# Performance work log

Hardware: AMD Instinct MI355X
Metric: run time of the kernel (lower is better)

The kernel has to match this reference:

```python
import jax, jax.numpy as jnp
import numpy as np

N = 50000      # number of nodes (rows of edge_embeddings)
E = 800000     # number of edges
D = 256        # edge_dim
TOPK = 50


def setup_inputs() -> dict:
    key = jax.random.key(0)
    k1, k2, k3, k4, k5, k6 = jax.random.split(key, 6)
    edge_embeddings = jax.random.normal(k1, (N, D), dtype=jnp.float32)
    edge_index = jax.random.randint(k2, (2, E), 0, N, dtype=jnp.int64)
    # PyTorch nn.Linear default init: U(-1/sqrt(fan_in), 1/sqrt(fan_in))
    s1 = 1.0 / np.sqrt(2 * D)
    s2 = 1.0 / np.sqrt(D)
    W1 = jax.random.uniform(k3, (2 * D, D), jnp.float32, -s1, s1)
    b1 = jax.random.uniform(k4, (D,), jnp.float32, -s1, s1)
    W2 = jax.random.uniform(k5, (D, 1), jnp.float32, -s2, s2)
    b2 = jax.random.uniform(k6, (1,), jnp.float32, -s2, s2)
    return {"edge_embeddings": edge_embeddings, "W1": W1, "b1": b1,
            "W2": W2, "b2": b2, "edge_index": edge_index, "top_k": TOPK}


def reference(edge_embeddings, W1, b1, W2, b2, edge_index, top_k):
    src, dst = edge_index[0], edge_index[1]           # [E]
    valid = src < dst                                  # original keeps only i<j pairs
    # gather + concat: [E, 2D]
    pair_emb = jnp.concatenate([edge_embeddings[src], edge_embeddings[dst]], axis=-1)
    h = jax.nn.relu(pair_emb @ W1 + b1)                # [E, D]
    score = jax.nn.sigmoid(h @ W2 + b2)[:, 0]          # [E], in (0,1)
    # invalid edges get score -1 (< any sigmoid output) so topk picks only valid ones
    masked = jnp.where(valid, score, jnp.float32(-1.0))
    top_scores, top_idx = jax.lax.top_k(masked, top_k)
    top_pairs = edge_index[:, top_idx]                 # [2, k] (src,dst) of top edges
    return top_pairs, top_scores
```

## Files before the change

kernel.cpp:

```cpp
#include <hip/hip_runtime.h>
#include <hip/hip_bf16.h>
#include <cstdint>

#define TOPK 50
#define CANDS 400
#define HIST_BINS 16384
#define CAND_CAP 16384
#define NFBLK 512
#define SORT_CAP 8192

typedef __attribute__((ext_vector_type(8))) short bf16x8;
typedef __attribute__((ext_vector_type(4))) float f32x4;

__device__ __forceinline__ unsigned short f2bf(float f) {
    unsigned u = __float_as_uint(f);
    u += 0x7FFFu + ((u >> 16) & 1u);
    return (unsigned short)(u >> 16);
}

__global__ __launch_bounds__(256) void prep_kernel(const float* __restrict__ W1,
                                                   unsigned* __restrict__ Wcf4,
                                                   unsigned* __restrict__ hist,
                                                   unsigned* __restrict__ misc,
                                                   const int* __restrict__ eidx) {
    int g = blockIdx.x * blockDim.x + threadIdx.x;
    {
        int l = g & 63;
        int kt = (g >> 6) & 7;
        int nt = g >> 9;
        int col = nt * 16 + (l & 15);
        int kb = kt * 32 + (l >> 4) * 8;
        unsigned short h[8];
#pragma unroll
        for (int j = 0; j < 8; ++j) {
            int k = kb + j;
            float f = (col < 256) ? W1[k * 256 + col] : W1[(256 + k) * 256 + (col - 256)];
            h[j] = f2bf(f);
        }
        unsigned* dst = Wcf4 + (size_t)g * 4;
        dst[0] = (unsigned)h[0] | ((unsigned)h[1] << 16);
        dst[1] = (unsigned)h[2] | ((unsigned)h[3] << 16);
        dst[2] = (unsigned)h[4] | ((unsigned)h[5] << 16);
        dst[3] = (unsigned)h[6] | ((unsigned)h[7] << 16);
    }
    if (g < HIST_BINS) hist[g] = 0;
    if (g == 0) {
        int allz = 1;
        for (int q = 0; q < 64; ++q)
            if (eidx[2 * q + 1] != 0) { allz = 0; break; }
        misc[0] = (unsigned)allz;
        misc[2] = 0;
        misc[3] = 0;
        misc[4] = 0;
    }
}

__global__ __launch_bounds__(256) void gemm_fused(const float* __restrict__ emb,
                                                  const bf16x8* __restrict__ Bv,
                                                  const float* __restrict__ b1,
                                                  unsigned char* __restrict__ C8, int M) {
    __shared__ uint4 afrag[2048];
    const int t = threadIdx.x;
    const int w = t >> 6;
    const int l = t & 63;

    uint2* w2 = (uint2*)afrag;
#pragma unroll
    for (int iter = 0; iter < 16; ++iter) {
        int r = iter * 4 + w;
        int c0 = l * 4;
        int gr = blockIdx.x * 64 + r;
        float4 v = make_float4(0.f, 0.f, 0.f, 0.f);
        if (gr < M) v = *(const float4*)&emb[(size_t)gr * 256 + c0];
        unsigned u0 = (unsigned)f2bf(v.x) | ((unsigned)f2bf(v.y) << 16);
        unsigned u1 = (unsigned)f2bf(v.z) | ((unsigned)f2bf(v.w) << 16);
        int mt = r >> 4;
        int kt = c0 >> 5;
        int lane = (r & 15) + ((c0 & 31) >> 3) * 16;
        int f = mt * 8 + kt;
        int slot = f * 64 + (lane ^ (f & 7));
        w2[slot * 2 + ((c0 & 7) >> 2)] = make_uint2(u0, u1);
    }
    __syncthreads();

    const int wn = w;
#pragma unroll
    for (int nh = 0; nh < 2; ++nh) {
        f32x4 acc[4][4];
#pragma unroll
        for (int i = 0; i < 4; ++i)
#pragma unroll
            for (int j = 0; j < 4; ++j) acc[i][j] = (f32x4){0.f, 0.f, 0.f, 0.f};

        const int nt0 = wn * 8 + nh * 4;
        bf16x8 bcur[4];
#pragma unroll
        for (int j = 0; j < 4; ++j)
            bcur[j] = Bv[(size_t)((nt0 + j) * 8 + 0) * 64 + l];

#pragma unroll
        for (int kt = 0; kt < 8; ++kt) {
            bf16x8 af[4];
#pragma unroll
            for (int i = 0; i < 4; ++i)
                af[i] = *(const bf16x8*)&afrag[(i * 8 + kt) * 64 + (l ^ kt)];
            bf16x8 bnxt[4];
            if (kt < 7) {
#pragma unroll
                for (int j = 0; j < 4; ++j)
                    bnxt[j] = Bv[(size_t)((nt0 + j) * 8 + kt + 1) * 64 + l];
            }
#pragma unroll
            for (int i = 0; i < 4; ++i)
#pragma unroll
                for (int j = 0; j < 4; ++j)
                    acc[i][j] = __builtin_amdgcn_mfma_f32_16x16x32_bf16(af[i], bcur[j], acc[i][j], 0, 0, 0);
            if (kt < 7) {
#pragma unroll
                for (int j = 0; j < 4; ++j) bcur[j] = bnxt[j];
            }
        }

#pragma unroll
        for (int i = 0; i < 4; ++i) {
            int row0 = blockIdx.x * 64 + i * 16 + (l >> 4) * 4;
#pragma unroll
            for (int j = 0; j < 4; ++j) {
                int col = (nt0 + j) * 16 + (l & 15);
                float bias = (col < 256) ? b1[col] : 0.f;
#pragma unroll
                for (int r = 0; r < 4; ++r) {
                    float v = acc[i][j][r] + bias;
                    int pk = __builtin_amdgcn_cvt_pk_fp8_f32(v, v, 0, false);
                    C8[(size_t)(row0 + r) * 512 + col] = (unsigned char)(pk & 0xFF);
                }
            }
        }
    }
}

__global__ __launch_bounds__(256) void count_valid(const int* __restrict__ eidx,
                                                   const unsigned* __restrict__ misc,
                                                   unsigned* __restrict__ bcount, int E) {
    const int is64 = (int)misc[0];
    const int chunk = (E + gridDim.x - 1) / gridDim.x;
    const int lo = blockIdx.x * chunk;
    const int hi = min(E, lo + chunk);
    unsigned cnt = 0;
    for (int e = lo + threadIdx.x; e < hi; e += blockDim.x) {
        int s, d;
        if (is64) {
            s = ((const int2*)eidx)[e].x;
            d = ((const int2*)eidx)[(size_t)e + E].x;
        } else {
            s = eidx[e];
            d = eidx[e + E];
        }
        cnt += (s < d);
    }
#pragma unroll
    for (int off = 32; off; off >>= 1) cnt += __shfl_xor(cnt, off, 64);
    __shared__ unsigned wsum[4];
    if ((threadIdx.x & 63) == 0) wsum[threadIdx.x >> 6] = cnt;
    __syncthreads();
    if (threadIdx.x == 0)
        bcount[blockIdx.x] = wsum[0] + wsum[1] + wsum[2] + wsum[3];
}

__global__ __launch_bounds__(256) void scan_blocks(const unsigned* __restrict__ bcount,
                                                   unsigned* __restrict__ boffset,
                                                   unsigned* __restrict__ misc) {
    __shared__ unsigned sc[256];
    const int t = threadIdx.x;
    unsigned a = bcount[2 * t], b = bcount[2 * t + 1];
    sc[t] = a + b;
    __syncthreads();
    for (int off = 1; off < 256; off <<= 1) {
        unsigned v = (t >= off) ? sc[t - off] : 0u;
        __syncthreads();
        sc[t] += v;
        __syncthreads();
    }
    unsigned excl = sc[t] - (a + b);
    boffset[2 * t] = excl;
    boffset[2 * t + 1] = excl + a;
    if (t == 255) misc[4] = sc[255];
}

__global__ __launch_bounds__(256) void write_valid(const int* __restrict__ eidx,
                                                   const unsigned* __restrict__ misc,
                                                   const unsigned* __restrict__ boffset,
                                                   int* __restrict__ vsrc,
                                                   int* __restrict__ vdst,
                                                   int* __restrict__ vid, int E) {
    const int is64 = (int)misc[0];
    const int chunk = (E + gridDim.x - 1) / gridDim.x;
    const int lo = blockIdx.x * chunk;
    const int hi = min(E, lo + chunk);
    const int lane = threadIdx.x & 63;
    const int w = threadIdx.x >> 6;
    __shared__ unsigned wcnt[4];
    unsigned running = boffset[blockIdx.x];
    for (int base = lo; base < hi; base += blockDim.x) {
        int e = base + threadIdx.x;
        bool valid = false;
        int s = 0, d = 0;
        if (e < hi) {
            if (is64) {
                s = ((const int2*)eidx)[e].x;
                d = ((const int2*)eidx)[(size_t)e + E].x;
            } else {
                s = eidx[e];
                d = eidx[e + E];
            }
            valid = s < d;
        }
        unsigned long long m = __ballot(valid);
        unsigned pfx = __popcll(m & ((1ull << lane) - 1ull));
        if (lane == 0) wcnt[w] = __popcll(m);
        __syncthreads();
        unsigned wbase = running;
        for (int i = 0; i < w; ++i) wbase += wcnt[i];
        if (valid) {
            unsigned p = wbase + pfx;
            vsrc[p] = s;
            vdst[p] = d;
            vid[p] = e;
        }
        unsigned tot = wcnt[0] + wcnt[1] + wcnt[2] + wcnt[3];
        __syncthreads();
        running += tot;
    }
}

__device__ __forceinline__ float dotq(unsigned a, unsigned b, float4 w) {
    float s;
    s  = fmaxf(__builtin_amdgcn_cvt_f32_fp8(a, 0) + __builtin_amdgcn_cvt_f32_fp8(b, 0), 0.f) * w.x;
    s += fmaxf(__builtin_amdgcn_cvt_f32_fp8(a, 1) + __builtin_amdgcn_cvt_f32_fp8(b, 1), 0.f) * w.y;
    s += fmaxf(__builtin_amdgcn_cvt_f32_fp8(a, 2) + __builtin_amdgcn_cvt_f32_fp8(b, 2), 0.f) * w.z;
    s += fmaxf(__builtin_amdgcn_cvt_f32_fp8(a, 3) + __builtin_amdgcn_cvt_f32_fp8(b, 3), 0.f) * w.w;
    return s;
}

__global__ __launch_bounds__(256) void edge_score_fp8(const unsigned char* __restrict__ C8,
                                                      const int* __restrict__ vsrc,
                                                      const int* __restrict__ vdst,
                                                      const float* __restrict__ W2,
                                                      const float* __restrict__ b2,
                                                      float* __restrict__ svals,
                                                      const unsigned* __restrict__ misc) {
    const int V = (int)misc[4];
    const int lane = threadIdx.x & 63;
    const int q = lane & 15;
    const int g = lane >> 4;
    const int wid = blockIdx.x * (blockDim.x >> 6) + (threadIdx.x >> 6);
    const int nw = gridDim.x * (blockDim.x >> 6);

    const float4 w0 = *(const float4*)&W2[q * 16 + 0];
    const float4 w1 = *(const float4*)&W2[q * 16 + 4];
    const float4 w2 = *(const float4*)&W2[q * 16 + 8];
    const float4 w3 = *(const float4*)&W2[q * 16 + 12];
    const float bb2 = b2[0];

    for (int base = wid * 4; base < V; base += nw * 4) {
        const int slot = base + g;
        const bool ok = slot < V;
        const int src = ok ? vsrc[slot] : 0;
        const int dst = ok ? vdst[slot] : 0;
        const uint4 ua = *(const uint4*)(C8 + (size_t)src * 512 + q * 16);
        const uint4 ub = *(const uint4*)(C8 + (size_t)dst * 512 + 256 + q * 16);
        float p = dotq(ua.x, ub.x, w0);
        p += dotq(ua.y, ub.y, w1);
        p += dotq(ua.z, ub.z, w2);
        p += dotq(ua.w, ub.w, w3);
        p += __shfl_xor(p, 1, 64);
        p += __shfl_xor(p, 2, 64);
        p += __shfl_xor(p, 4, 64);
        p += __shfl_xor(p, 8, 64);
        if (q == 0 && ok) {
            float z = p + bb2;
            float sc = 1.0f / (1.0f + expf(-z));
            svals[slot] = sc;
        }
    }
}

__global__ __launch_bounds__(256) void hist_kernel(const float* __restrict__ svals,
                                                   const unsigned* __restrict__ misc,
                                                   unsigned* __restrict__ hist) {
    __shared__ unsigned lh[HIST_BINS];
    const int V = (int)misc[4];
    const int t = threadIdx.x;
    for (int i = t; i < HIST_BINS; i += 256) lh[i] = 0;
    __syncthreads();
    int i = blockIdx.x * blockDim.x + t;
    int stride = gridDim.x * blockDim.x;
    for (int v = i; v < V; v += stride)
        atomicAdd(&lh[__float_as_uint(svals[v]) >> 16], 1u);
    __syncthreads();
    for (int b = t; b < HIST_BINS; b += 256) {
        unsigned c = lh[b];
        if (c) atomicAdd(&hist[b], c);
    }
}

__global__ void scan_hist(const unsigned* __restrict__ hist, unsigned* __restrict__ misc) {
    __shared__ unsigned chunk[256];
    int t = threadIdx.x;
    unsigned s = 0;
    for (int i = 0; i < 64; ++i) s += hist[t * 64 + i];
    chunk[t] = s;
    __syncthreads();
    if (t == 0) {
        unsigned cum = 0;
        int c;
        unsigned thr = 0;
        for (c = 255; c >= 0; --c) {
            if (cum + chunk[c] >= CANDS) break;
            cum += chunk[c];
        }
        if (c >= 0) {
            for (int b = c * 64 + 63; b >= c * 64; --b) {
                cum += hist[b];
                if (cum >= CANDS) { thr = ((unsigned)b) << 16; break; }
            }
        }
        misc[2] = thr;
    }
}

__global__ void compact(const float* __restrict__ svals, const int* __restrict__ vid,
                        unsigned* __restrict__ misc,
                        unsigned long long* __restrict__ cand) {
    const int V = (int)misc[4];
    const unsigned thr = misc[2];
    int i = blockIdx.x * blockDim.x + threadIdx.x;
    int stride = gridDim.x * blockDim.x;
    for (int v = i; v < V; v += stride) {
        unsigned bits = __float_as_uint(svals[v]);
        if (bits >= thr) {
            unsigned pos = atomicAdd(&misc[3], 1u);
            if (pos < CAND_CAP)
                cand[pos] = ((unsigned long long)bits << 32) |
                            (unsigned)(0xFFFFFFFFu - (unsigned)vid[v]);
        }
    }
}

__global__ __launch_bounds__(256) void rescore(const float* __restrict__ emb,
                                               const float* __restrict__ W1,
                                               const float* __restrict__ b1,
                                               const float* __restrict__ W2,
                                               const float* __restrict__ b2,
                                               const int* __restrict__ eidx,
                                               const unsigned long long* __restrict__ cand,
                                               const unsigned* __restrict__ misc,
                                               unsigned long long* __restrict__ rescored,
                                               int E) {
    __shared__ float es[256], ed[256];
    __shared__ float red[256];
    const int C = (int)min(misc[3], (unsigned)CAND_CAP);
    const int is64 = (int)misc[0];
    const int t = threadIdx.x;
    for (int c = blockIdx.x; c < C; c += gridDim.x) {
        unsigned long long entry = cand[c];
        unsigned e = 0xFFFFFFFFu - (unsigned)(entry & 0xFFFFFFFFu);
        int src, dst;
        if (is64) {
            src = eidx[2 * (size_t)e];
            dst = eidx[2 * ((size_t)e + E)];
        } else {
            src = eidx[e];
            dst = eidx[e + E];
        }
        es[t] = emb[(size_t)src * 256 + t];
        ed[t] = emb[(size_t)dst * 256 + t];
        __syncthreads();
        float h = b1[t];
#pragma unroll 8
        for (int k = 0; k < 256; ++k) h += es[k] * W1[k * 256 + t];
#pragma unroll 8
        for (int k = 0; k < 256; ++k) h += ed[k] * W1[(256 + k) * 256 + t];
        red[t] = fmaxf(h, 0.f) * W2[t];
        __syncthreads();
        for (int s = 128; s; s >>= 1) {
            if (t < s) red[t] += red[t + s];
            __syncthreads();
        }
        if (t == 0) {
            float z = red[0] + b2[0];
            float sc = 1.0f / (1.0f + expf(-z));
            rescored[c] = ((unsigned long long)__float_as_uint(sc) << 32) |
                          (unsigned)(0xFFFFFFFFu - e);
        }
        __syncthreads();
    }
}

__global__ __launch_bounds__(256) void final_topk(unsigned long long* __restrict__ rescored,
                                                  const unsigned* __restrict__ misc,
                                                  const int* __restrict__ eidx,
                                                  float* __restrict__ out, int E) {
    __shared__ unsigned long long a[SORT_CAP];
    const int t = threadIdx.x;
    const int C = (int)min(misc[3], (unsigned)CAND_CAP);
    const int is64 = (int)misc[0];

    if (C <= SORT_CAP) {
        int n = 256;
        while (n < C) n <<= 1;
        for (int i = t; i < n; i += 256) a[i] = (i < C) ? rescored[i] : 0ull;
        __syncthreads();
        for (int k = 2; k <= n; k <<= 1) {
            for (int j = k >> 1; j > 0; j >>= 1) {
                for (int i = t; i < n; i += 256) {
                    int ixj = i ^ j;
                    if (ixj > i) {
                        unsigned long long x = a[i], y = a[ixj];
                        bool sw = ((i & k) == 0) ? (x < y) : (x > y);
                        if (sw) { a[i] = y; a[ixj] = x; }
                    }
                }
                __syncthreads();
            }
        }
        if (t < TOPK) {
            unsigned long long m = a[t];
            if (m != 0ull) {
                unsigned bits = (unsigned)(m >> 32);
                unsigned e = 0xFFFFFFFFu - (unsigned)(m & 0xFFFFFFFFu);
                int src, dst;
                if (is64) {
                    src = eidx[2 * (size_t)e];
                    dst = eidx[2 * ((size_t)e + E)];
                } else {
                    src = eidx[e];
                    dst = eidx[e + E];
                }
                out[t] = (float)src;
                out[TOPK + t] = (float)dst;
                out[2 * TOPK + t] = __uint_as_float(bits);
            } else {
                out[t] = -1.f;
                out[TOPK + t] = -1.f;
                out[2 * TOPK + t] = -1.f;
            }
        }
        return;
    }

    __shared__ unsigned long long red[256];
    for (int r = 0; r < TOPK; ++r) {
        unsigned long long best = 0ull;
        for (int i = t; i < C; i += 256) {
            unsigned long long v = rescored[i];
            if (v > best) best = v;
        }
        red[t] = best;
        __syncthreads();
        for (int s = 128; s; s >>= 1) {
            if (t < s) {
                if (red[t + s] > red[t]) red[t] = red[t + s];
            }
            __syncthreads();
        }
        unsigned long long m = red[0];
        __syncthreads();
        for (int i = t; i < C; i += 256)
            if (rescored[i] == m) rescored[i] = 0ull;
        if (t == 0) {
            if (m != 0ull) {
                unsigned bits = (unsigned)(m >> 32);
                unsigned e = 0xFFFFFFFFu - (unsigned)(m & 0xFFFFFFFFu);
                int src, dst;
                if (is64) {
                    src = eidx[2 * (size_t)e];
                    dst = eidx[2 * ((size_t)e + E)];
                } else {
                    src = eidx[e];
                    dst = eidx[e + E];
                }
                out[r] = (float)src;
                out[TOPK + r] = (float)dst;
                out[2 * TOPK + r] = __uint_as_float(bits);
            } else {
                out[r] = -1.f;
                out[TOPK + r] = -1.f;
                out[2 * TOPK + r] = -1.f;
            }
        }
        __syncthreads();
    }
}

extern "C" void kernel_launch(void* const* d_in, const int* in_sizes, int n_in,
                              void* d_out, int out_size, void* d_ws, size_t ws_size,
                              hipStream_t stream) {
    const float* emb = (const float*)d_in[0];
    const float* W1  = (const float*)d_in[1];
    const float* b1  = (const float*)d_in[2];
    const float* W2  = (const float*)d_in[3];
    const float* b2  = (const float*)d_in[4];
    const int*   eidx = (const int*)d_in[5];

    const int M = in_sizes[0] / 256;
    const int E = in_sizes[5] / 2;
    const int Mpad = ((M + 63) / 64) * 64;

    char* p = (char*)d_ws;
    auto alloc = [&](size_t bytes) {
        char* r = p;
        p += (bytes + 255) & ~(size_t)255;
        return r;
    };
    unsigned* Wcf4 = (unsigned*)alloc(256 * 512 * 2);
    unsigned char* C8 = (unsigned char*)alloc((size_t)Mpad * 512);
    float* svals = (float*)alloc((size_t)E * 4);
    int* vsrc = (int*)alloc((size_t)E * 4);
    int* vdst = (int*)alloc((size_t)E * 4);
    int* vid  = (int*)alloc((size_t)E * 4);
    unsigned* hist = (unsigned*)alloc(HIST_BINS * 4);
    unsigned long long* cand = (unsigned long long*)alloc(CAND_CAP * 8);
    unsigned long long* resc = (unsigned long long*)alloc(CAND_CAP * 8);
    unsigned* bcount = (unsigned*)alloc(NFBLK * 4);
    unsigned* boffset = (unsigned*)alloc(NFBLK * 4);
    unsigned* misc = (unsigned*)alloc(256);

    float* out = (float*)d_out;

    prep_kernel<<<64, 256, 0, stream>>>(W1, Wcf4, hist, misc, eidx);

    gemm_fused<<<Mpad / 64, 256, 0, stream>>>(emb, (const bf16x8*)Wcf4, b1, C8, M);

    count_valid<<<NFBLK, 256, 0, stream>>>(eidx, misc, bcount, E);
    scan_blocks<<<1, 256, 0, stream>>>(bcount, boffset, misc);
    write_valid<<<NFBLK, 256, 0, stream>>>(eidx, misc, boffset, vsrc, vdst, vid, E);

    edge_score_fp8<<<2048, 256, 0, stream>>>(C8, vsrc, vdst, W2, b2, svals, misc);

    hist_kernel<<<128, 256, 0, stream>>>(svals, misc, hist);

    scan_hist<<<1, 256, 0, stream>>>(hist, misc);

    compact<<<1024, 256, 0, stream>>>(svals, vid, misc, cand);

    rescore<<<1024, 256, 0, stream>>>(emb, W1, b1, W2, b2, eidx, cand, misc, resc, E);

    final_topk<<<1, 256, 0, stream>>>(resc, misc, eidx, out, E);
}
```

Before: 154.9 us.

## Replace LDS-staged node GEMM with single-wave register-resident A fragments

```diff
diff --git a/kernel.cpp b/kernel.cpp
--- a/kernel.cpp
+++ b/kernel.cpp
@@ -55,66 +55,63 @@
     }
 }
 
-__global__ __launch_bounds__(256) void gemm_fused(const float* __restrict__ emb,
-                                                  const bf16x8* __restrict__ Bv,
-                                                  const float* __restrict__ b1,
-                                                  unsigned char* __restrict__ C8, int M) {
-    __shared__ uint4 afrag[2048];
-    const int t = threadIdx.x;
-    const int w = t >> 6;
-    const int l = t & 63;
-
-    uint2* w2 = (uint2*)afrag;
-#pragma unroll
-    for (int iter = 0; iter < 16; ++iter) {
-        int r = iter * 4 + w;
-        int c0 = l * 4;
-        int gr = blockIdx.x * 64 + r;
-        float4 v = make_float4(0.f, 0.f, 0.f, 0.f);
-        if (gr < M) v = *(const float4*)&emb[(size_t)gr * 256 + c0];
-        unsigned u0 = (unsigned)f2bf(v.x) | ((unsigned)f2bf(v.y) << 16);
-        unsigned u1 = (unsigned)f2bf(v.z) | ((unsigned)f2bf(v.w) << 16);
-        int mt = r >> 4;
-        int kt = c0 >> 5;
-        int lane = (r & 15) + ((c0 & 31) >> 3) * 16;
-        int f = mt * 8 + kt;
-        int slot = f * 64 + (lane ^ (f & 7));
-        w2[slot * 2 + ((c0 & 7) >> 2)] = make_uint2(u0, u1);
-    }
-    __syncthreads();
-
-    const int wn = w;
-#pragma unroll
-    for (int nh = 0; nh < 2; ++nh) {
+__global__ __launch_bounds__(64) void gemm_reg(const float* __restrict__ emb,
+                                               const bf16x8* __restrict__ Bv,
+                                               const float* __restrict__ b1,
+                                               unsigned char* __restrict__ C8, int M) {
+    const int l = threadIdx.x;
+    const int row0 = blockIdx.x * 64;
+    const int kq = (l >> 4) * 8;
+
+    bf16x8 af[4][8];
+#pragma unroll
+    for (int mt = 0; mt < 4; ++mt) {
+        int gr = row0 + mt * 16 + (l & 15);
+        bool ok = gr < M;
+        const float* rp = &emb[(size_t)(ok ? gr : 0) * 256 + kq];
+#pragma unroll
+        for (int kt = 0; kt < 8; ++kt) {
+            float4 v0 = make_float4(0.f, 0.f, 0.f, 0.f);
+            float4 v1 = v0;
+            if (ok) {
+                v0 = *(const float4*)&rp[kt * 32];
+                v1 = *(const float4*)&rp[kt * 32 + 4];
+            }
+            unsigned q0 = (unsigned)f2bf(v0.x) | ((unsigned)f2bf(v0.y) << 16);
+            unsigned q1 = (unsigned)f2bf(v0.z) | ((unsigned)f2bf(v0.w) << 16);
+            unsigned q2 = (unsigned)f2bf(v1.x) | ((unsigned)f2bf(v1.y) << 16);
+            unsigned q3 = (unsigned)f2bf(v1.z) | ((unsigned)f2bf(v1.w) << 16);
+            uint4 u = make_uint4(q0, q1, q2, q3);
+            af[mt][kt] = *(bf16x8*)&u;
+        }
+    }
+
+#pragma unroll 1
+    for (int nq = 0; nq < 8; ++nq) {
         f32x4 acc[4][4];
 #pragma unroll
         for (int i = 0; i < 4; ++i)
 #pragma unroll
             for (int j = 0; j < 4; ++j) acc[i][j] = (f32x4){0.f, 0.f, 0.f, 0.f};
 
-        const int nt0 = wn * 8 + nh * 4;
         bf16x8 bcur[4];
 #pragma unroll
         for (int j = 0; j < 4; ++j)
-            bcur[j] = Bv[(size_t)((nt0 + j) * 8 + 0) * 64 + l];
+            bcur[j] = Bv[(size_t)((nq * 4 + j) * 8 + 0) * 64 + l];
 
 #pragma unroll
         for (int kt = 0; kt < 8; ++kt) {
-            bf16x8 af[4];
-#pragma unroll
-            for (int i = 0; i < 4; ++i)
-                af[i] = *(const bf16x8*)&afrag[(i * 8 + kt) * 64 + (l ^ kt)];
             bf16x8 bnxt[4];
             if (kt < 7) {
 #pragma unroll
                 for (int j = 0; j < 4; ++j)
-                    bnxt[j] = Bv[(size_t)((nt0 + j) * 8 + kt + 1) * 64 + l];
+                    bnxt[j] = Bv[(size_t)((nq * 4 + j) * 8 + kt + 1) * 64 + l];
             }
 #pragma unroll
             for (int i = 0; i < 4; ++i)
 #pragma unroll
                 for (int j = 0; j < 4; ++j)
-                    acc[i][j] = __builtin_amdgcn_mfma_f32_16x16x32_bf16(af[i], bcur[j], acc[i][j], 0, 0, 0);
+                    acc[i][j] = __builtin_amdgcn_mfma_f32_16x16x32_bf16(af[i][kt], bcur[j], acc[i][j], 0, 0, 0);
             if (kt < 7) {
 #pragma unroll
                 for (int j = 0; j < 4; ++j) bcur[j] = bnxt[j];
@@ -123,16 +120,16 @@
 
 #pragma unroll
         for (int i = 0; i < 4; ++i) {
-            int row0 = blockIdx.x * 64 + i * 16 + (l >> 4) * 4;
+            int r0 = row0 + i * 16 + (l >> 4) * 4;
 #pragma unroll
             for (int j = 0; j < 4; ++j) {
-                int col = (nt0 + j) * 16 + (l & 15);
+                int col = (nq * 4 + j) * 16 + (l & 15);
                 float bias = (col < 256) ? b1[col] : 0.f;
 #pragma unroll
-                for (int r = 0; r < 4; ++r) {
-                    float v = acc[i][j][r] + bias;
+                for (int rr = 0; rr < 4; ++rr) {
+                    float v = acc[i][j][rr] + bias;
                     int pk = __builtin_amdgcn_cvt_pk_fp8_f32(v, v, 0, false);
-                    C8[(size_t)(row0 + r) * 512 + col] = (unsigned char)(pk & 0xFF);
+                    C8[(size_t)(r0 + rr) * 512 + col] = (unsigned char)(pk & 0xFF);
                 }
             }
         }
@@ -530,7 +527,7 @@
 
     prep_kernel<<<64, 256, 0, stream>>>(W1, Wcf4, hist, misc, eidx);
 
-    gemm_fused<<<Mpad / 64, 256, 0, stream>>>(emb, (const bf16x8*)Wcf4, b1, C8, M);
+    gemm_reg<<<Mpad / 64, 64, 0, stream>>>(emb, (const bf16x8*)Wcf4, b1, C8, M);
 
     count_valid<<<NFBLK, 256, 0, stream>>>(eidx, misc, bcount, E);
     scan_blocks<<<1, 256, 0, stream>>>(bcount, boffset, misc);
```

Measured after the change: 170.2 us. 1.1x slower.

## Fuse block scan into write_valid and histogram into edge scoring

Applied to the files above, without the earlier changes.

```diff
diff --git a/kernel.cpp b/kernel.cpp
--- a/kernel.cpp
+++ b/kernel.cpp
@@ -167,42 +167,44 @@
         bcount[blockIdx.x] = wsum[0] + wsum[1] + wsum[2] + wsum[3];
 }
 
-__global__ __launch_bounds__(256) void scan_blocks(const unsigned* __restrict__ bcount,
-                                                   unsigned* __restrict__ boffset,
-                                                   unsigned* __restrict__ misc) {
-    __shared__ unsigned sc[256];
+__global__ __launch_bounds__(256) void write_valid_scan(const int* __restrict__ eidx,
+                                                        unsigned* __restrict__ misc,
+                                                        const unsigned* __restrict__ bcount,
+                                                        int* __restrict__ vsrc,
+                                                        int* __restrict__ vdst,
+                                                        int* __restrict__ vid, int E) {
+    const int is64 = (int)misc[0];
+    const int bid = blockIdx.x;
     const int t = threadIdx.x;
-    unsigned a = bcount[2 * t], b = bcount[2 * t + 1];
-    sc[t] = a + b;
-    __syncthreads();
-    for (int off = 1; off < 256; off <<= 1) {
-        unsigned v = (t >= off) ? sc[t - off] : 0u;
-        __syncthreads();
-        sc[t] += v;
-        __syncthreads();
-    }
-    unsigned excl = sc[t] - (a + b);
-    boffset[2 * t] = excl;
-    boffset[2 * t + 1] = excl + a;
-    if (t == 255) misc[4] = sc[255];
-}
-
-__global__ __launch_bounds__(256) void write_valid(const int* __restrict__ eidx,
-                                                   const unsigned* __restrict__ misc,
-                                                   const unsigned* __restrict__ boffset,
-                                                   int* __restrict__ vsrc,
-                                                   int* __restrict__ vdst,
-                                                   int* __restrict__ vid, int E) {
-    const int is64 = (int)misc[0];
+    __shared__ unsigned red[256];
+
+    unsigned c0 = bcount[t], c1 = bcount[t + 256];
+    unsigned pa = ((t < bid) ? c0 : 0u) + ((t + 256 < bid) ? c1 : 0u);
+    red[t] = pa;
+    __syncthreads();
+    for (int s = 128; s; s >>= 1) {
+        if (t < s) red[t] += red[t + s];
+        __syncthreads();
+    }
+    const unsigned myoff = red[0];
+    __syncthreads();
+    red[t] = c0 + c1;
+    __syncthreads();
+    for (int s = 128; s; s >>= 1) {
+        if (t < s) red[t] += red[t + s];
+        __syncthreads();
+    }
+    if (bid == 0 && t == 0) misc[4] = red[0];
+
     const int chunk = (E + gridDim.x - 1) / gridDim.x;
-    const int lo = blockIdx.x * chunk;
+    const int lo = bid * chunk;
     const int hi = min(E, lo + chunk);
-    const int lane = threadIdx.x & 63;
-    const int w = threadIdx.x >> 6;
+    const int lane = t & 63;
+    const int w = t >> 6;
     __shared__ unsigned wcnt[4];
-    unsigned running = boffset[blockIdx.x];
+    unsigned running = myoff;
     for (int base = lo; base < hi; base += blockDim.x) {
-        int e = base + threadIdx.x;
+        int e = base + t;
         bool valid = false;
         int s = 0, d = 0;
         if (e < hi) {
@@ -248,12 +250,18 @@
                                                       const float* __restrict__ W2,
                                                       const float* __restrict__ b2,
                                                       float* __restrict__ svals,
+                                                      unsigned* __restrict__ hist,
                                                       const unsigned* __restrict__ misc) {
+    __shared__ unsigned lh[HIST_BINS / 2];
     const int V = (int)misc[4];
-    const int lane = threadIdx.x & 63;
+    const int t = threadIdx.x;
+    for (int i = t; i < HIST_BINS / 2; i += 256) lh[i] = 0;
+    __syncthreads();
+
+    const int lane = t & 63;
     const int q = lane & 15;
     const int g = lane >> 4;
-    const int wid = blockIdx.x * (blockDim.x >> 6) + (threadIdx.x >> 6);
+    const int wid = blockIdx.x * (blockDim.x >> 6) + (t >> 6);
     const int nw = gridDim.x * (blockDim.x >> 6);
 
     const float4 w0 = *(const float4*)&W2[q * 16 + 0];
@@ -281,26 +289,16 @@
             float z = p + bb2;
             float sc = 1.0f / (1.0f + expf(-z));
             svals[slot] = sc;
-        }
-    }
-}
-
-__global__ __launch_bounds__(256) void hist_kernel(const float* __restrict__ svals,
-                                                   const unsigned* __restrict__ misc,
-                                                   unsigned* __restrict__ hist) {
-    __shared__ unsigned lh[HIST_BINS];
-    const int V = (int)misc[4];
-    const int t = threadIdx.x;
-    for (int i = t; i < HIST_BINS; i += 256) lh[i] = 0;
-    __syncthreads();
-    int i = blockIdx.x * blockDim.x + t;
-    int stride = gridDim.x * blockDim.x;
-    for (int v = i; v < V; v += stride)
-        atomicAdd(&lh[__float_as_uint(svals[v]) >> 16], 1u);
-    __syncthreads();
-    for (int b = t; b < HIST_BINS; b += 256) {
-        unsigned c = lh[b];
-        if (c) atomicAdd(&hist[b], c);
+            unsigned b = __float_as_uint(sc) >> 16;
+            atomicAdd(&lh[b >> 1], 1u << ((b & 1) * 16));
+        }
+    }
+    __syncthreads();
+    for (int i = t; i < HIST_BINS / 2; i += 256) {
+        unsigned v = lh[i];
+        unsigned lo = v & 0xFFFFu, hi = v >> 16;
+        if (lo) atomicAdd(&hist[2 * i], lo);
+        if (hi) atomicAdd(&hist[2 * i + 1], hi);
     }
 }
 
@@ -523,7 +521,6 @@
     unsigned long long* cand = (unsigned long long*)alloc(CAND_CAP * 8);
     unsigned long long* resc = (unsigned long long*)alloc(CAND_CAP * 8);
     unsigned* bcount = (unsigned*)alloc(NFBLK * 4);
-    unsigned* boffset = (unsigned*)alloc(NFBLK * 4);
     unsigned* misc = (unsigned*)alloc(256);
 
     float* out = (float*)d_out;
@@ -533,12 +530,9 @@
     gemm_fused<<<Mpad / 64, 256, 0, stream>>>(emb, (const bf16x8*)Wcf4, b1, C8, M);
 
     count_valid<<<NFBLK, 256, 0, stream>>>(eidx, misc, bcount, E);
-    scan_blocks<<<1, 256, 0, stream>>>(bcount, boffset, misc);
-    write_valid<<<NFBLK, 256, 0, stream>>>(eidx, misc, boffset, vsrc, vdst, vid, E);
-
-    edge_score_fp8<<<2048, 256, 0, stream>>>(C8, vsrc, vdst, W2, b2, svals, misc);
-
-    hist_kernel<<<128, 256, 0, stream>>>(svals, misc, hist);
+    write_valid_scan<<<NFBLK, 256, 0, stream>>>(eidx, misc, bcount, vsrc, vdst, vid, E);
+
+    edge_score_fp8<<<2048, 256, 0, stream>>>(C8, vsrc, vdst, W2, b2, svals, hist, misc);
 
     scan_hist<<<1, 256, 0, stream>>>(hist, misc);
 
```

New measurement: 215.8 us. 1.39x slower.
